# Optimization experiments

Measured on AMD Instinct MI355X. Metric: run time of the kernel, lower is better.

## Reference

```python
import jax, jax.numpy as jnp
import numpy as np

EPS = 1e-5  # BatchNorm eps (torch default)

def setup_inputs() -> dict:
    key = jax.random.key(0)
    ks = jax.random.split(key, 12)
    B, C, H, W = 4, 256, 64, 64
    IC = 128  # inter_channels = C // 2
    s = 1.0 / np.sqrt(C)
    si = 1.0 / np.sqrt(IC)
    return {
        "x": jax.random.normal(ks[0], (B, C, H, W), jnp.float32),
        "y": jax.random.normal(ks[1], (B, C, H, W), jnp.float32),
        "g_w": jax.random.normal(ks[2], (IC, C), jnp.float32) * s,
        "g_b": jax.random.normal(ks[3], (IC,), jnp.float32) * 0.01,
        "dx_w": jax.random.normal(ks[4], (IC, C), jnp.float32) * s,
        "dx_b": jax.random.normal(ks[5], (IC,), jnp.float32) * 0.01,
        "dy_w": jax.random.normal(ks[6], (IC, C), jnp.float32) * s,
        "dy_b": jax.random.normal(ks[7], (IC,), jnp.float32) * 0.01,
        "w_w": jax.random.normal(ks[8], (C, IC), jnp.float32) * si,
        "w_b": jax.random.normal(ks[9], (C,), jnp.float32) * 0.01,
        "bn_gamma": jax.random.normal(ks[10], (C,), jnp.float32),
        "bn_beta": jax.random.normal(ks[11], (C,), jnp.float32) * 0.01,
    }

def _conv1x1(t, w, b):
    # t: [B,C,H,W], w: [O,C], b: [O] -> [B,O,H,W]
    return jnp.einsum('bchw,oc->bohw', t, w) + b[None, :, None, None]

def reference(x, y, g_w, g_b, dx_w, dx_b, dy_w, dy_b, w_w, w_b, bn_gamma, bn_beta):
    B, C, H, W = x.shape
    IC = g_w.shape[0]
    N = H * W
    g_y = _conv1x1(y, g_w, g_b).reshape(B, IC, N).transpose(0, 2, 1)      # [B,N,IC]
    theta_x = _conv1x1(x, dx_w, dx_b).reshape(B, IC, N).transpose(0, 2, 1)  # [B,N,IC]
    phi_y = _conv1x1(y, dy_w, dy_b).reshape(B, IC, N)                      # [B,IC,N]
    f = jnp.einsum('bnc,bcm->bnm', theta_x, phi_y)                         # [B,N,N]
    f_div_C = jax.nn.softmax(f, axis=-1)
    y2 = jnp.einsum('bnm,bmc->bnc', f_div_C, g_y)                          # [B,N,IC]
    y2 = y2.transpose(0, 2, 1).reshape(B, IC, H, W)
    wy = _conv1x1(y2, w_w, w_b)                                            # [B,C,H,W]
    # BatchNorm2d in training mode: batch stats over (B,H,W) per channel
    mean = jnp.mean(wy, axis=(0, 2, 3), keepdims=True)
    var = jnp.var(wy, axis=(0, 2, 3), keepdims=True)
    wy_bn = (wy - mean) / jnp.sqrt(var + EPS)
    wy_bn = wy_bn * bn_gamma[None, :, None, None] + bn_beta[None, :, None, None]
    return wy_bn + x
```

## Files before the change

### kernel.cpp

```cpp
#include <hip/hip_runtime.h>
#include <hip/hip_bf16.h>
#include <math.h>

typedef unsigned short ushort_t;
typedef __attribute__((ext_vector_type(8))) short     short8;
typedef __attribute__((ext_vector_type(8))) _Float16  half8;
typedef __attribute__((ext_vector_type(8))) unsigned short ushort8;
typedef __attribute__((ext_vector_type(4))) float     float4v;
typedef __attribute__((ext_vector_type(16))) float    floatx16;

__device__ __forceinline__ float b2f(ushort_t u) {
    return __uint_as_float(((unsigned)u) << 16);
}
__device__ __forceinline__ ushort_t f2b(float f) {
    unsigned i = __float_as_uint(f);
    return (ushort_t)((i + 0x7FFFu + ((i >> 16) & 1u)) >> 16);
}
__device__ __forceinline__ void split2(float v, ushort_t& h, ushort_t& l) {
    h = f2b(v);
    l = f2b(v - b2f(h));
}
__device__ __forceinline__ void glds16(const ushort_t* g, ushort_t* l) {
    __builtin_amdgcn_global_load_lds((const __attribute__((address_space(1))) void*)g,
                                     (__attribute__((address_space(3))) void*)l, 16, 0, 0);
}
__device__ __forceinline__ unsigned int pack2bf(float lo, float hi) {
    unsigned int r;
    asm("v_cvt_pk_bf16_f32 %0, %1, %2" : "=v"(r) : "v"(lo), "v"(hi));
    return r;
}
__device__ __forceinline__ void pl32swap(unsigned int& a, unsigned int& b) {
    asm("v_permlane32_swap_b32 %0, %1" : "+v"(a), "+v"(b));
}

#define WTFH_OFF   0
#define WTFL_OFF   196608
#define WWBH_OFF   393216
#define WWBL_OFF   458752
#define BIAS_OFF   524288
#define PROJF_OFF  1048576
#define GT_OFF     9437184
#define OPART_OFF  13631488
#define WY_OFF     1048576
#define PART_OFF   9437184

__global__ void prep_k(const float* __restrict__ dx_w, const float* __restrict__ dy_w,
                       const float* __restrict__ g_w,  const float* __restrict__ dx_b,
                       const float* __restrict__ dy_b, const float* __restrict__ g_b,
                       const float* __restrict__ w_w,
                       ushort_t* __restrict__ wtfh, ushort_t* __restrict__ wtfl,
                       ushort_t* __restrict__ wwbh, ushort_t* __restrict__ wwbl,
                       float* __restrict__ bias) {
    int idx = blockIdx.x * 256 + threadIdx.x;
    int j = idx & 7, lane = (idx >> 3) & 63, kk = (idx >> 9) & 7, ot = idx >> 12;
    int o = ot * 16 + (lane & 15);
    int c = kk * 32 + ((lane >> 4) * 8) + j;
    float v;
    if (o < 128)      v = dx_w[o * 256 + c];
    else if (o < 256) v = dy_w[(o - 128) * 256 + c];
    else              v = g_w[(o - 256) * 256 + c];
    ushort_t h, l;
    split2(v, h, l);
    wtfh[idx] = h; wtfl[idx] = l;
    if (idx < 32768) {
        split2(w_w[idx], h, l);
        wwbh[idx] = h; wwbl[idx] = l;
    }
    if (idx < 384) {
        bias[idx] = (idx < 128) ? dx_b[idx]
                  : (idx < 256) ? dy_b[idx - 128]
                                : g_b[idx - 256];
    }
}

#define XTS 258
__global__ __launch_bounds__(256) void proj_k(const float* __restrict__ x,
                                              const float* __restrict__ y,
                                              const ushort_t* __restrict__ wtfh,
                                              const ushort_t* __restrict__ wtfl,
                                              const float* __restrict__ bias,
                                              ushort_t* __restrict__ projf,
                                              ushort_t* __restrict__ gT) {
    __shared__ ushort_t xT[2][32 * XTS];
    int b = blockIdx.y, n0 = blockIdx.x * 32;
    int s = blockIdx.z;
    int tid = threadIdx.x;
    int w = tid >> 6, lane = tid & 63;
    int mrow = lane & 15, quad = lane >> 4, koff = quad * 8;
    int half = w & 1, sect = w >> 1;
    int arow = half * 16 + mrow;

    const float* src = s ? y : x;
    #pragma unroll
    for (int i = 0; i < 4; i++) {
        int ch = tid + i * 256;
        int c = ch >> 2, off = (ch & 3) * 8;
        const float* p = src + (size_t)(b * 256 + c) * 4096 + n0 + off;
        float4v v0 = *(const float4v*)p;
        float4v v1 = *(const float4v*)(p + 4);
        #pragma unroll
        for (int jj = 0; jj < 4; jj++) {
            ushort_t h, l;
            split2(v0[jj], h, l);
            xT[0][(off + jj) * XTS + c] = h;
            xT[1][(off + jj) * XTS + c] = l;
            split2(v1[jj], h, l);
            xT[0][(off + 4 + jj) * XTS + c] = h;
            xT[1][(off + 4 + jj) * XTS + c] = l;
        }
    }
    __syncthreads();

    short8 fh[8], fl[8];
    #pragma unroll
    for (int kk = 0; kk < 8; kk++) {
        fh[kk] = *(const short8*)&xT[0][arow * XTS + kk * 32 + koff];
        fl[kk] = *(const short8*)&xT[1][arow * XTS + kk * 32 + koff];
    }

    int ot0 = s ? (8 + sect * 8) : (sect * 4);
    int ot1 = s ? (ot0 + 8) : (ot0 + 4);
    for (int ot = ot0; ot < ot1; ot++) {
        float4v acc = {0.f, 0.f, 0.f, 0.f};
        #pragma unroll
        for (int kk = 0; kk < 8; kk++) {
            short8 bh = *(const short8*)(wtfh + (size_t)((ot * 8 + kk) * 64 + lane) * 8);
            short8 bl = *(const short8*)(wtfl + (size_t)((ot * 8 + kk) * 64 + lane) * 8);
            acc = __builtin_amdgcn_mfma_f32_16x16x32_bf16(fh[kk], bh, acc, 0, 0, 0);
            acc = __builtin_amdgcn_mfma_f32_16x16x32_bf16(fh[kk], bl, acc, 0, 0, 0);
            acc = __builtin_amdgcn_mfma_f32_16x16x32_bf16(fl[kk], bh, acc, 0, 0, 0);
        }
        int o = ot * 16 + mrow;
        float bo = bias[o];
        #pragma unroll
        for (int r = 0; r < 4; r++) {
            int n = n0 + half * 16 + quad * 4 + r;
            float v = acc[r] + bo;
            if (ot < 16) {
                _Float16 hf = (_Float16)v;
                projf[(size_t)(b * 4096 + n) * 256 + o] = *(ushort_t*)&hf;
            } else {
                gT[(size_t)(b * 128 + (o - 256)) * 4096 + n] = f2b(v);
            }
        }
    }
}

template<int KVB>
__global__ __launch_bounds__(256, (KVB == 32 ? 4 : 2))
void flash_k(const ushort_t* __restrict__ projf,
             const ushort_t* __restrict__ gT,
             float* __restrict__ opart,
             float* __restrict__ oml,
             int kqlog) {
    constexpr int NT2 = KVB / 32;
    constexpr int NCH = KVB / 4;
    constexpr int NPT = NCH / 4;
    __shared__ __align__(16) ushort_t KsF[2][KVB * 128];
    __shared__ __align__(16) ushort_t VsF[2][KVB * 128];

    int L = blockIdx.x;
    int xcd = L & 7, t = L >> 3;
    int c, j;
    if (kqlog >= 2)      { c = (t >> 5) * 8 + xcd; j = t & 31; }
    else if (kqlog == 1) { c = xcd;                j = t; }
    else                 { c = xcd & 3;            j = t + ((xcd >> 2) << 4); }
    int b  = c >> kqlog;
    int kq = c & ((1 << kqlog) - 1);
    int q0 = j * 128;
    int iters = (4096 >> kqlog) / KVB;
    int kt0 = kq * iters;
    int tid = threadIdx.x, w = tid >> 6, lane = tid & 63;
    int ln = lane & 31, hh = lane >> 5;

    const ushort_t* kSrc[NPT];
    const ushort_t* vSrc[NPT];
    {
        int kb0 = kt0 * KVB;
        #pragma unroll
        for (int i = 0; i < NPT; i++) {
            int cc = w + i * 4;
            int t2 = cc >> 3, kk = cc & 7;
            kSrc[i] = projf + (size_t)(b * 4096 + kb0 + t2 * 32 + ln) * 256 + 128 + kk * 16 + hh * 8;
            int it = cc / (2 * NT2), g = cc % (2 * NT2);
            vSrc[i] = gT + (size_t)(b * 128 + it * 32 + ln) * 4096 + kb0 + g * 16 + hh * 8;
        }
    }

    half8 qf[8];
    {
        const ushort_t* qp = projf + (size_t)(b * 4096 + q0 + w * 32 + ln) * 256 + hh * 8;
        #pragma unroll
        for (int kk = 0; kk < 8; kk++)
            qf[kk] = *(const half8*)(qp + kk * 16);
    }

    floatx16 oacc[4];
    #pragma unroll
    for (int it = 0; it < 4; it++)
        #pragma unroll
        for (int jj = 0; jj < 16; jj++) oacc[it][jj] = 0.f;
    float lacc[NT2];
    #pragma unroll
    for (int t2 = 0; t2 < NT2; t2++) lacc[t2] = 0.f;

    #pragma unroll
    for (int i = 0; i < NPT; i++) {
        int cc = w + i * 4;
        glds16(kSrc[i], &KsF[0][cc * 512]);
        glds16(vSrc[i], &VsF[0][cc * 512]);
        kSrc[i] += (size_t)KVB * 256;
        vSrc[i] += KVB;
    }

    for (int kt = kt0; kt < kt0 + iters; kt++) {
        int cur = (kt - kt0) & 1;
        __syncthreads();
        if (kt + 1 < kt0 + iters) {
            #pragma unroll
            for (int i = 0; i < NPT; i++) {
                int cc = w + i * 4;
                glds16(kSrc[i], &KsF[1 - cur][cc * 512]);
                glds16(vSrc[i], &VsF[1 - cur][cc * 512]);
                kSrc[i] += (size_t)KVB * 256;
                vSrc[i] += KVB;
            }
        }

        floatx16 sacc[NT2];
        #pragma unroll
        for (int t2 = 0; t2 < NT2; t2++)
            #pragma unroll
            for (int jj = 0; jj < 16; jj++) sacc[t2][jj] = 0.f;
        __builtin_amdgcn_s_setprio(1);
        #pragma unroll
        for (int kk = 0; kk < 8; kk++) {
            #pragma unroll
            for (int t2 = 0; t2 < NT2; t2++) {
                half8 ah = *(const half8*)&KsF[cur][((t2 * 8 + kk) * 64 + lane) * 8];
                sacc[t2] = __builtin_amdgcn_mfma_f32_32x32x16_f16(ah, qf[kk], sacc[t2], 0, 0, 0);
            }
        }
        __builtin_amdgcn_s_setprio(0);

        short8 fr[2 * NT2];
        #pragma unroll
        for (int t2 = 0; t2 < NT2; t2++) {
            float ps[16];
            #pragma unroll
            for (int r = 0; r < 16; r++)
                ps[r] = __builtin_exp2f(fmaf(sacc[t2][r], 1.44269504f, -92.332481f));
            lacc[t2] += ((((ps[0] + ps[1]) + (ps[2] + ps[3]))
                        + ((ps[4] + ps[5]) + (ps[6] + ps[7])))
                       + (((ps[8] + ps[9]) + (ps[10] + ps[11]))
                        + ((ps[12] + ps[13]) + (ps[14] + ps[15]))));
            unsigned int pw[8];
            #pragma unroll
            for (int c2 = 0; c2 < 8; c2++) pw[c2] = pack2bf(ps[2 * c2], ps[2 * c2 + 1]);
            pl32swap(pw[0], pw[2]);
            pl32swap(pw[1], pw[3]);
            pl32swap(pw[4], pw[6]);
            pl32swap(pw[5], pw[7]);
            union { unsigned int u[4]; short8 s8; } fA, fB;
            fA.u[0] = pw[0]; fA.u[1] = pw[1]; fA.u[2] = pw[2]; fA.u[3] = pw[3];
            fB.u[0] = pw[4]; fB.u[1] = pw[5]; fB.u[2] = pw[6]; fB.u[3] = pw[7];
            fr[t2 * 2]     = fA.s8;
            fr[t2 * 2 + 1] = fB.s8;
        }

        __builtin_amdgcn_s_setprio(1);
        #pragma unroll
        for (int it = 0; it < 4; it++) {
            #pragma unroll
            for (int kg = 0; kg < 2 * NT2; kg++) {
                short8 vv = *(const short8*)&VsF[cur][((it * 2 * NT2 + kg) * 64 + lane) * 8];
                oacc[it] = __builtin_amdgcn_mfma_f32_32x32x16_bf16(fr[kg], vv, oacc[it], 0, 0, 0);
            }
        }
        __builtin_amdgcn_s_setprio(0);
    }

    {
        int rowBase = b * 4096 + q0 + w * 32 + hh * 4;
        #pragma unroll
        for (int it = 0; it < 4; it++)
            #pragma unroll
            for (int r = 0; r < 16; r++) {
                int qrow = rowBase + (r & 3) + 8 * (r >> 2);
                opart[((size_t)kq * 16384 + qrow) * 128 + it * 32 + ln] = oacc[it][r];
            }
    }
    float lsum = lacc[0];
    #pragma unroll
    for (int t2 = 1; t2 < NT2; t2++) lsum += lacc[t2];
    lsum += __shfl_xor(lsum, 32, 64);
    if (lane < 32)
        oml[kq * 16384 + b * 4096 + q0 + w * 32 + lane] = lsum;
}

template<int KQ>
__global__ __launch_bounds__(256) void wy_k(const float* __restrict__ opart,
                                            const float* __restrict__ oml,
                                            const ushort_t* __restrict__ wwbh,
                                            const ushort_t* __restrict__ wwbl,
                                            const float* __restrict__ w_b,
                                            ushort_t* __restrict__ wy,
                                            float* __restrict__ part) {
    int b = blockIdx.y, n0 = blockIdx.x * 32;
    int tid = threadIdx.x, w = tid >> 6, lane = tid & 63;
    int mrow = lane & 15, quad = lane >> 4, koff = quad * 8;
    int half = w & 1, sect = w >> 1;
    int Rn = b * 4096 + n0 + half * 16 + mrow;

    float L = 0.f;
    #pragma unroll
    for (int kq = 0; kq < KQ; kq++) L += oml[kq * 16384 + Rn];
    float invL = 1.f / L;

    short8 bfh[4], bfl[4];
    #pragma unroll
    for (int kk = 0; kk < 4; kk++) {
        float a[8];
        #pragma unroll
        for (int j = 0; j < 8; j++) a[j] = 0.f;
        #pragma unroll
        for (int kq = 0; kq < KQ; kq++) {
            const float* p = opart + ((size_t)kq * 16384 + Rn) * 128 + kk * 32 + koff;
            float4v v0 = *(const float4v*)p;
            float4v v1 = *(const float4v*)(p + 4);
            #pragma unroll
            for (int j = 0; j < 4; j++) { a[j] += v0[j]; a[4 + j] += v1[j]; }
        }
        #pragma unroll
        for (int j = 0; j < 8; j++) {
            ushort_t h, l;
            split2(a[j] * invL, h, l);
            bfh[kk][j] = (short)h; bfl[kk][j] = (short)l;
        }
    }

    int coln = n0 + half * 16 + mrow;
    int pcol = (blockIdx.x * 4 + b) * 2 + half;
    for (int cot = sect * 8; cot < sect * 8 + 8; cot++) {
        float4v acc = {0.f, 0.f, 0.f, 0.f};
        #pragma unroll
        for (int kk = 0; kk < 4; kk++) {
            size_t woff = (size_t)(cot * 16 + mrow) * 128 + kk * 32 + koff;
            short8 ah = *(const short8*)(wwbh + woff);
            short8 al = *(const short8*)(wwbl + woff);
            acc = __builtin_amdgcn_mfma_f32_16x16x32_bf16(ah, bfh[kk], acc, 0, 0, 0);
            acc = __builtin_amdgcn_mfma_f32_16x16x32_bf16(ah, bfl[kk], acc, 0, 0, 0);
            acc = __builtin_amdgcn_mfma_f32_16x16x32_bf16(al, bfh[kk], acc, 0, 0, 0);
        }
        float s1v[4], s2v[4];
        #pragma unroll
        for (int r = 0; r < 4; r++) {
            int co = cot * 16 + quad * 4 + r;
            ushort_t bv = f2b(acc[r] + w_b[co]);
            wy[(size_t)(b * 256 + co) * 4096 + coln] = bv;
            float vb = b2f(bv);
            s1v[r] = vb; s2v[r] = vb * vb;
        }
        #pragma unroll
        for (int d = 1; d < 16; d <<= 1) {
            #pragma unroll
            for (int r = 0; r < 4; r++) {
                s1v[r] += __shfl_xor(s1v[r], d, 64);
                s2v[r] += __shfl_xor(s2v[r], d, 64);
            }
        }
        if (mrow == 0) {
            #pragma unroll
            for (int r = 0; r < 4; r++) {
                int co = cot * 16 + quad * 4 + r;
                part[co * 1024 + pcol]          = s1v[r];
                part[262144 + co * 1024 + pcol] = s2v[r];
            }
        }
    }
}

__global__ __launch_bounds__(256) void bn_k(const ushort_t* __restrict__ wy,
                                            const float* __restrict__ x,
                                            const float* __restrict__ gamma,
                                            const float* __restrict__ beta,
                                            const float* __restrict__ part,
                                            float* __restrict__ out) {
    __shared__ float red[8];
    __shared__ float sc[2];
    int tid = threadIdx.x, w = tid >> 6, lane = tid & 63;
    int idx = (blockIdx.x * 256 + tid) * 8;
    int c = (idx >> 12) & 255;

    float4v p1 = *(const float4v*)(part + c * 1024 + tid * 4);
    float4v p2 = *(const float4v*)(part + 262144 + c * 1024 + tid * 4);
    float s  = (p1[0] + p1[1]) + (p1[2] + p1[3]);
    float s2 = (p2[0] + p2[1]) + (p2[2] + p2[3]);
    #pragma unroll
    for (int d = 1; d < 64; d <<= 1) { s += __shfl_xor(s, d, 64); s2 += __shfl_xor(s2, d, 64); }
    if (lane == 0) { red[w] = s; red[4 + w] = s2; }
    __syncthreads();
    if (tid == 0) {
        float S  = (red[0] + red[1]) + (red[2] + red[3]);
        float S2 = (red[4] + red[5]) + (red[6] + red[7]);
        const float inv_cnt = 1.f / 16384.f;
        float mean = S * inv_cnt;
        float var  = S2 * inv_cnt - mean * mean;
        float inv  = rsqrtf(var + 1e-5f);
        float scale = gamma[c] * inv;
        sc[0] = scale;
        sc[1] = beta[c] - mean * scale;
    }
    __syncthreads();
    float scale = sc[0], shift = sc[1];

    ushort8 wv = *(const ushort8*)(wy + idx);
    float4v x0 = *(const float4v*)(x + idx);
    float4v x1 = *(const float4v*)(x + idx + 4);
    float4v o0, o1;
    #pragma unroll
    for (int j = 0; j < 4; j++) {
        o0[j] = b2f(wv[j]) * scale + shift + x0[j];
        o1[j] = b2f(wv[4 + j]) * scale + shift + x1[j];
    }
    *(float4v*)(out + idx) = o0;
    *(float4v*)(out + idx + 4) = o1;
}

extern "C" void kernel_launch(void* const* d_in, const int* in_sizes, int n_in,
                              void* d_out, int out_size, void* d_ws, size_t ws_size,
                              hipStream_t stream) {
    const float* x    = (const float*)d_in[0];
    const float* y    = (const float*)d_in[1];
    const float* g_w  = (const float*)d_in[2];
    const float* g_b  = (const float*)d_in[3];
    const float* dx_w = (const float*)d_in[4];
    const float* dx_b = (const float*)d_in[5];
    const float* dy_w = (const float*)d_in[6];
    const float* dy_b = (const float*)d_in[7];
    const float* w_w  = (const float*)d_in[8];
    const float* w_b  = (const float*)d_in[9];
    const float* bn_g = (const float*)d_in[10];
    const float* bn_b = (const float*)d_in[11];

    char* ws = (char*)d_ws;
    ushort_t* wtfh  = (ushort_t*)(ws + WTFH_OFF);
    ushort_t* wtfl  = (ushort_t*)(ws + WTFL_OFF);
    ushort_t* wwbh  = (ushort_t*)(ws + WWBH_OFF);
    ushort_t* wwbl  = (ushort_t*)(ws + WWBL_OFF);
    float*    bias  = (float*)(ws + BIAS_OFF);
    ushort_t* projf = (ushort_t*)(ws + PROJF_OFF);
    ushort_t* gT    = (ushort_t*)(ws + GT_OFF);
    float*    opart = (float*)(ws + OPART_OFF);
    ushort_t* wy    = (ushort_t*)(ws + WY_OFF);
    float*    part  = (float*)(ws + PART_OFF);
    float*    out   = (float*)d_out;

    int kqlog;
    if      (ws_size >= 13631488u + 4u * (8388608u + 65536u)) kqlog = 2;
    else if (ws_size >= 13631488u + 2u * (8388608u + 65536u)) kqlog = 1;
    else                                                      kqlog = 0;
    int KQ = 1 << kqlog;
    float* oml = (float*)(ws + OPART_OFF + (size_t)KQ * 8388608u);

    prep_k<<<384, 256, 0, stream>>>(dx_w, dy_w, g_w, dx_b, dy_b, g_b, w_w,
                                    wtfh, wtfl, wwbh, wwbl, bias);
    proj_k<<<dim3(128, 4, 2), 256, 0, stream>>>(x, y, wtfh, wtfl, bias, projf, gT);
    flash_k<64><<<dim3(128 << kqlog), 256, 0, stream>>>(projf, gT, opart, oml, kqlog);
    if (KQ == 4)
        wy_k<4><<<dim3(128, 4), 256, 0, stream>>>(opart, oml, wwbh, wwbl, w_b, wy, part);
    else if (KQ == 2)
        wy_k<2><<<dim3(128, 4), 256, 0, stream>>>(opart, oml, wwbh, wwbl, w_b, wy, part);
    else
        wy_k<1><<<dim3(128, 4), 256, 0, stream>>>(opart, oml, wwbh, wwbl, w_b, wy, part);
    bn_k<<<2048, 256, 0, stream>>>(wy, x, bn_g, bn_b, part, out);
}
```

Before: 207.1 us.

## Fuse output projection and BatchNorm apply with a grid-wide atomic barrier

```diff
diff --git a/kernel.cpp b/kernel.cpp
--- a/kernel.cpp
+++ b/kernel.cpp
@@ -38,6 +38,7 @@
 #define WWBH_OFF   393216
 #define WWBL_OFF   458752
 #define BIAS_OFF   524288
+#define BAR_OFF    526336
 #define PROJF_OFF  1048576
 #define GT_OFF     9437184
 #define OPART_OFF  13631488
@@ -50,7 +51,7 @@
                        const float* __restrict__ w_w,
                        ushort_t* __restrict__ wtfh, ushort_t* __restrict__ wtfl,
                        ushort_t* __restrict__ wwbh, ushort_t* __restrict__ wwbl,
-                       float* __restrict__ bias) {
+                       float* __restrict__ bias, int* __restrict__ bar) {
     int idx = blockIdx.x * 256 + threadIdx.x;
     int j = idx & 7, lane = (idx >> 3) & 63, kk = (idx >> 9) & 7, ot = idx >> 12;
     int o = ot * 16 + (lane & 15);
@@ -71,6 +72,7 @@
                   : (idx < 256) ? dy_b[idx - 128]
                                 : g_b[idx - 256];
     }
+    if (idx == 0) *bar = 0;
 }
 
 #define XTS 258
@@ -299,132 +301,146 @@
 }
 
 template<int KQ>
-__global__ __launch_bounds__(256) void wy_k(const float* __restrict__ opart,
-                                            const float* __restrict__ oml,
-                                            const ushort_t* __restrict__ wwbh,
-                                            const ushort_t* __restrict__ wwbl,
-                                            const float* __restrict__ w_b,
-                                            ushort_t* __restrict__ wy,
-                                            float* __restrict__ part) {
-    int b = blockIdx.y, n0 = blockIdx.x * 32;
+__global__ __launch_bounds__(256) void wybn_k(const float* __restrict__ opart,
+                                              const float* __restrict__ oml,
+                                              const ushort_t* __restrict__ wwbh,
+                                              const ushort_t* __restrict__ wwbl,
+                                              const float* __restrict__ w_b,
+                                              ushort_t* __restrict__ wy,
+                                              float* __restrict__ part,
+                                              const float* __restrict__ x,
+                                              const float* __restrict__ gamma,
+                                              const float* __restrict__ beta,
+                                              float* __restrict__ out,
+                                              int* __restrict__ bar) {
+    __shared__ float red[8];
+    __shared__ float sc[2];
+    int bid = blockIdx.x;
+    int b = bid >> 7, n0 = (bid & 127) * 32;
     int tid = threadIdx.x, w = tid >> 6, lane = tid & 63;
     int mrow = lane & 15, quad = lane >> 4, koff = quad * 8;
     int half = w & 1, sect = w >> 1;
-    int Rn = b * 4096 + n0 + half * 16 + mrow;
-
-    float L = 0.f;
-    #pragma unroll
-    for (int kq = 0; kq < KQ; kq++) L += oml[kq * 16384 + Rn];
-    float invL = 1.f / L;
-
-    short8 bfh[4], bfl[4];
-    #pragma unroll
-    for (int kk = 0; kk < 4; kk++) {
-        float a[8];
-        #pragma unroll
-        for (int j = 0; j < 8; j++) a[j] = 0.f;
-        #pragma unroll
-        for (int kq = 0; kq < KQ; kq++) {
-            const float* p = opart + ((size_t)kq * 16384 + Rn) * 128 + kk * 32 + koff;
-            float4v v0 = *(const float4v*)p;
-            float4v v1 = *(const float4v*)(p + 4);
-            #pragma unroll
-            for (int j = 0; j < 4; j++) { a[j] += v0[j]; a[4 + j] += v1[j]; }
-        }
-        #pragma unroll
-        for (int j = 0; j < 8; j++) {
-            ushort_t h, l;
-            split2(a[j] * invL, h, l);
-            bfh[kk][j] = (short)h; bfl[kk][j] = (short)l;
-        }
-    }
-
-    int coln = n0 + half * 16 + mrow;
-    int pcol = (blockIdx.x * 4 + b) * 2 + half;
-    for (int cot = sect * 8; cot < sect * 8 + 8; cot++) {
-        float4v acc = {0.f, 0.f, 0.f, 0.f};
+
+    {
+        int Rn = b * 4096 + n0 + half * 16 + mrow;
+        float L = 0.f;
+        #pragma unroll
+        for (int kq = 0; kq < KQ; kq++) L += oml[kq * 16384 + Rn];
+        float invL = 1.f / L;
+
+        short8 bfh[4], bfl[4];
         #pragma unroll
         for (int kk = 0; kk < 4; kk++) {
-            size_t woff = (size_t)(cot * 16 + mrow) * 128 + kk * 32 + koff;
-            short8 ah = *(const short8*)(wwbh + woff);
-            short8 al = *(const short8*)(wwbl + woff);
-            acc = __builtin_amdgcn_mfma_f32_16x16x32_bf16(ah, bfh[kk], acc, 0, 0, 0);
-            acc = __builtin_amdgcn_mfma_f32_16x16x32_bf16(ah, bfl[kk], acc, 0, 0, 0);
-            acc = __builtin_amdgcn_mfma_f32_16x16x32_bf16(al, bfh[kk], acc, 0, 0, 0);
-        }
-        float s1v[4], s2v[4];
-        #pragma unroll
-        for (int r = 0; r < 4; r++) {
-            int co = cot * 16 + quad * 4 + r;
-            ushort_t bv = f2b(acc[r] + w_b[co]);
-            wy[(size_t)(b * 256 + co) * 4096 + coln] = bv;
-            float vb = b2f(bv);
-            s1v[r] = vb; s2v[r] = vb * vb;
-        }
-        #pragma unroll
-        for (int d = 1; d < 16; d <<= 1) {
-            #pragma unroll
-            for (int r = 0; r < 4; r++) {
-                s1v[r] += __shfl_xor(s1v[r], d, 64);
-                s2v[r] += __shfl_xor(s2v[r], d, 64);
-            }
-        }
-        if (mrow == 0) {
+            float a[8];
+            #pragma unroll
+            for (int j = 0; j < 8; j++) a[j] = 0.f;
+            #pragma unroll
+            for (int kq = 0; kq < KQ; kq++) {
+                const float* p = opart + ((size_t)kq * 16384 + Rn) * 128 + kk * 32 + koff;
+                float4v v0 = *(const float4v*)p;
+                float4v v1 = *(const float4v*)(p + 4);
+                #pragma unroll
+                for (int j = 0; j < 4; j++) { a[j] += v0[j]; a[4 + j] += v1[j]; }
+            }
+            #pragma unroll
+            for (int j = 0; j < 8; j++) {
+                ushort_t h, l;
+                split2(a[j] * invL, h, l);
+                bfh[kk][j] = (short)h; bfl[kk][j] = (short)l;
+            }
+        }
+
+        int coln = n0 + half * 16 + mrow;
+        int pcol = ((bid & 127) * 4 + b) * 2 + half;
+        for (int cot = sect * 8; cot < sect * 8 + 8; cot++) {
+            float4v acc = {0.f, 0.f, 0.f, 0.f};
+            #pragma unroll
+            for (int kk = 0; kk < 4; kk++) {
+                size_t woff = (size_t)(cot * 16 + mrow) * 128 + kk * 32 + koff;
+                short8 ah = *(const short8*)(wwbh + woff);
+                short8 al = *(const short8*)(wwbl + woff);
+                acc = __builtin_amdgcn_mfma_f32_16x16x32_bf16(ah, bfh[kk], acc, 0, 0, 0);
+                acc = __builtin_amdgcn_mfma_f32_16x16x32_bf16(ah, bfl[kk], acc, 0, 0, 0);
+                acc = __builtin_amdgcn_mfma_f32_16x16x32_bf16(al, bfh[kk], acc, 0, 0, 0);
+            }
+            float s1v[4], s2v[4];
             #pragma unroll
             for (int r = 0; r < 4; r++) {
                 int co = cot * 16 + quad * 4 + r;
-                part[co * 1024 + pcol]          = s1v[r];
-                part[262144 + co * 1024 + pcol] = s2v[r];
-            }
-        }
-    }
-}
-
-__global__ __launch_bounds__(256) void bn_k(const ushort_t* __restrict__ wy,
-                                            const float* __restrict__ x,
-                                            const float* __restrict__ gamma,
-                                            const float* __restrict__ beta,
-                                            const float* __restrict__ part,
-                                            float* __restrict__ out) {
-    __shared__ float red[8];
-    __shared__ float sc[2];
-    int tid = threadIdx.x, w = tid >> 6, lane = tid & 63;
-    int idx = (blockIdx.x * 256 + tid) * 8;
-    int c = (idx >> 12) & 255;
-
-    float4v p1 = *(const float4v*)(part + c * 1024 + tid * 4);
-    float4v p2 = *(const float4v*)(part + 262144 + c * 1024 + tid * 4);
-    float s  = (p1[0] + p1[1]) + (p1[2] + p1[3]);
-    float s2 = (p2[0] + p2[1]) + (p2[2] + p2[3]);
-    #pragma unroll
-    for (int d = 1; d < 64; d <<= 1) { s += __shfl_xor(s, d, 64); s2 += __shfl_xor(s2, d, 64); }
-    if (lane == 0) { red[w] = s; red[4 + w] = s2; }
+                ushort_t bv = f2b(acc[r] + w_b[co]);
+                wy[(size_t)(b * 256 + co) * 4096 + coln] = bv;
+                float vb = b2f(bv);
+                s1v[r] = vb; s2v[r] = vb * vb;
+            }
+            #pragma unroll
+            for (int d = 1; d < 16; d <<= 1) {
+                #pragma unroll
+                for (int r = 0; r < 4; r++) {
+                    s1v[r] += __shfl_xor(s1v[r], d, 64);
+                    s2v[r] += __shfl_xor(s2v[r], d, 64);
+                }
+            }
+            if (mrow == 0) {
+                #pragma unroll
+                for (int r = 0; r < 4; r++) {
+                    int co = cot * 16 + quad * 4 + r;
+                    part[co * 1024 + pcol]          = s1v[r];
+                    part[262144 + co * 1024 + pcol] = s2v[r];
+                }
+            }
+        }
+    }
+
     __syncthreads();
     if (tid == 0) {
-        float S  = (red[0] + red[1]) + (red[2] + red[3]);
-        float S2 = (red[4] + red[5]) + (red[6] + red[7]);
-        const float inv_cnt = 1.f / 16384.f;
-        float mean = S * inv_cnt;
-        float var  = S2 * inv_cnt - mean * mean;
-        float inv  = rsqrtf(var + 1e-5f);
-        float scale = gamma[c] * inv;
-        sc[0] = scale;
-        sc[1] = beta[c] - mean * scale;
+        __threadfence();
+        atomicAdd(bar, 1);
+        while (atomicAdd(bar, 0) < (int)gridDim.x)
+            __builtin_amdgcn_s_sleep(8);
+        __threadfence();
     }
     __syncthreads();
-    float scale = sc[0], shift = sc[1];
-
-    ushort8 wv = *(const ushort8*)(wy + idx);
-    float4v x0 = *(const float4v*)(x + idx);
-    float4v x1 = *(const float4v*)(x + idx + 4);
-    float4v o0, o1;
-    #pragma unroll
-    for (int j = 0; j < 4; j++) {
-        o0[j] = b2f(wv[j]) * scale + shift + x0[j];
-        o1[j] = b2f(wv[4 + j]) * scale + shift + x1[j];
-    }
-    *(float4v*)(out + idx) = o0;
-    *(float4v*)(out + idx + 4) = o1;
+
+    for (int i = 0; i < 4; i++) {
+        int v = bid * 4 + i;
+        int idx = (v * 256 + tid) * 8;
+        int c = (idx >> 12) & 255;
+
+        float4v p1 = *(const float4v*)(part + c * 1024 + tid * 4);
+        float4v p2 = *(const float4v*)(part + 262144 + c * 1024 + tid * 4);
+        float s  = (p1[0] + p1[1]) + (p1[2] + p1[3]);
+        float s2 = (p2[0] + p2[1]) + (p2[2] + p2[3]);
+        #pragma unroll
+        for (int d = 1; d < 64; d <<= 1) { s += __shfl_xor(s, d, 64); s2 += __shfl_xor(s2, d, 64); }
+        if (lane == 0) { red[w] = s; red[4 + w] = s2; }
+        __syncthreads();
+        if (tid == 0) {
+            float S  = (red[0] + red[1]) + (red[2] + red[3]);
+            float S2 = (red[4] + red[5]) + (red[6] + red[7]);
+            const float inv_cnt = 1.f / 16384.f;
+            float mean = S * inv_cnt;
+            float var  = S2 * inv_cnt - mean * mean;
+            float inv  = rsqrtf(var + 1e-5f);
+            float scale = gamma[c] * inv;
+            sc[0] = scale;
+            sc[1] = beta[c] - mean * scale;
+        }
+        __syncthreads();
+        float scale = sc[0], shift = sc[1];
+
+        ushort8 wv = *(const ushort8*)(wy + idx);
+        float4v x0 = *(const float4v*)(x + idx);
+        float4v x1 = *(const float4v*)(x + idx + 4);
+        float4v o0, o1;
+        #pragma unroll
+        for (int j = 0; j < 4; j++) {
+            o0[j] = b2f(wv[j]) * scale + shift + x0[j];
+            o1[j] = b2f(wv[4 + j]) * scale + shift + x1[j];
+        }
+        *(float4v*)(out + idx) = o0;
+        *(float4v*)(out + idx + 4) = o1;
+        __syncthreads();
+    }
 }
 
 extern "C" void kernel_launch(void* const* d_in, const int* in_sizes, int n_in,
@@ -449,6 +465,7 @@
     ushort_t* wwbh  = (ushort_t*)(ws + WWBH_OFF);
     ushort_t* wwbl  = (ushort_t*)(ws + WWBL_OFF);
     float*    bias  = (float*)(ws + BIAS_OFF);
+    int*      bar   = (int*)(ws + BAR_OFF);
     ushort_t* projf = (ushort_t*)(ws + PROJF_OFF);
     ushort_t* gT    = (ushort_t*)(ws + GT_OFF);
     float*    opart = (float*)(ws + OPART_OFF);
@@ -464,14 +481,16 @@
     float* oml = (float*)(ws + OPART_OFF + (size_t)KQ * 8388608u);
 
     prep_k<<<384, 256, 0, stream>>>(dx_w, dy_w, g_w, dx_b, dy_b, g_b, w_w,
-                                    wtfh, wtfl, wwbh, wwbl, bias);
+                                    wtfh, wtfl, wwbh, wwbl, bias, bar);
     proj_k<<<dim3(128, 4, 2), 256, 0, stream>>>(x, y, wtfh, wtfl, bias, projf, gT);
     flash_k<64><<<dim3(128 << kqlog), 256, 0, stream>>>(projf, gT, opart, oml, kqlog);
     if (KQ == 4)
-        wy_k<4><<<dim3(128, 4), 256, 0, stream>>>(opart, oml, wwbh, wwbl, w_b, wy, part);
+        wybn_k<4><<<dim3(512), 256, 0, stream>>>(opart, oml, wwbh, wwbl, w_b, wy, part,
+                                                 x, bn_g, bn_b, out, bar);
     else if (KQ == 2)
-        wy_k<2><<<dim3(128, 4), 256, 0, stream>>>(opart, oml, wwbh, wwbl, w_b, wy, part);
+        wybn_k<2><<<dim3(512), 256, 0, stream>>>(opart, oml, wwbh, wwbl, w_b, wy, part,
+                                                 x, bn_g, bn_b, out, bar);
     else
-        wy_k<1><<<dim3(128, 4), 256, 0, stream>>>(opart, oml, wwbh, wwbl, w_b, wy, part);
-    bn_k<<<2048, 256, 0, stream>>>(wy, x, bn_g, bn_b, part, out);
-}
+        wybn_k<1><<<dim3(512), 256, 0, stream>>>(opart, oml, wwbh, wwbl, w_b, wy, part,
+                                                 x, bn_g, bn_b, out, bar);
+}
```

New measurement: 261.3 us. 1.26x slower.
